# Kernel tuning notes

Hardware: AMD Instinct MI355X
Metric: run time of the kernel (lower is better)

Reference implementation:

```python
import jax, jax.numpy as jnp
import numpy as np

ALPHA = 0.3
N_TAGS = 50  # POS tag vocabulary size (key space of the histogram)
B, S, R = 16, 160, 40


def setup_inputs() -> dict:
    key = jax.random.key(0)
    k1, k2, k3, k4, k5, k6 = jax.random.split(key, 6)
    return {
        "a_arc": jax.random.normal(k1, (B, S, S), dtype=jnp.float32),
        "a_rel": jax.random.normal(k2, (B, S, S, R), dtype=jnp.float32),
        "s_arc": jax.random.normal(k3, (B, S, S), dtype=jnp.float32),
        "s_rel": jax.random.normal(k4, (B, S, S, R), dtype=jnp.float32),
        "adds": jax.random.randint(k5, (B, S), 0, N_TAGS, dtype=jnp.int32),
        "pos": jax.random.randint(k6, (B, S), 0, N_TAGS, dtype=jnp.int32),
        "n_tags": N_TAGS,
    }


def reference(a_arc, a_rel, s_arc, s_rel, adds, pos, n_tags):
    # Histogram accumulation: score[(t1, t2)] += a_arc[i, p1, p2]
    # where t1 = adds[i, p1], t2 = adds[i, p2].  Flatten the pair key.
    R_ = a_rel.shape[-1]
    key_add = (adds[:, :, None] * n_tags + adds[:, None, :]).reshape(-1)  # [B*S*S]
    n_seg = n_tags * n_tags
    tab_arc = jax.ops.segment_sum(a_arc.reshape(-1), key_add, num_segments=n_seg)          # [T^2]
    tab_rel = jax.ops.segment_sum(a_rel.reshape(-1, R_), key_add, num_segments=n_seg)      # [T^2, R]
    # Gather back keyed on pos-tag pairs and blend with alpha.
    key_pos = pos[:, :, None] * n_tags + pos[:, None, :]  # [B, S, S]
    s_arc_out = s_arc + tab_arc[key_pos] * ALPHA
    s_rel_out = s_rel + tab_rel[key_pos] * ALPHA
    return s_arc_out, s_rel_out
```

## Files before the change

kernel.cpp:

```cpp
#include <hip/hip_runtime.h>

#define ALPHA 0.3f
#define NT    50
#define B_    16
#define S_    160
#define RR    40
#define Q_    (RR / 4)
#define NROW  (B_ * S_)
#define NPAIR (B_ * S_ * S_)
#define NSEG  (NT * NT)
#define NREL4 (NPAIR * Q_)
#define NCOL  (NT * RR + NT)
#define CW    2052

typedef float v4f __attribute__((ext_vector_type(4)));

__global__ void zero_tab(float* __restrict__ tab, int n) {
    int i = blockIdx.x * blockDim.x + threadIdx.x;
    if (i < n) tab[i] = 0.0f;
}

__global__ void build_lists(const int* __restrict__ adds,
                            int* __restrict__ colstart,
                            int* __restrict__ collist) {
    __shared__ int tags[S_];
    __shared__ int cnt[NT];
    __shared__ int start[NT + 1];
    int b   = blockIdx.x;
    int tid = threadIdx.x;
    if (tid < S_) tags[tid] = adds[b * S_ + tid];
    __syncthreads();
    if (tid < NT) {
        int c = 0;
        for (int i = 0; i < S_; i++) c += (tags[i] == tid);
        cnt[tid] = c;
    }
    __syncthreads();
    if (tid == 0) {
        int s = 0;
        for (int t = 0; t < NT; t++) { start[t] = s; s += cnt[t]; }
        start[NT] = s;
    }
    __syncthreads();
    if (tid <= NT) colstart[b * 64 + tid] = start[tid];
    if (tid < NT) {
        int slot = start[tid];
        for (int i = 0; i < S_; i++)
            if (tags[i] == tid) collist[b * S_ + slot++] = i;
    }
}

template <int TO_C>
__global__ __launch_bounds__(256) void stage1(const float* __restrict__ a_arc,
                                              const float4* __restrict__ a_rel4,
                                              const int* __restrict__ adds,
                                              const int* __restrict__ colstart,
                                              const int* __restrict__ collist,
                                              float* __restrict__ C,
                                              float* __restrict__ tab_arc,
                                              float* __restrict__ tab_rel) {
    __shared__ v4f   a_srt[S_ * Q_];
    __shared__ float aarc_srt[S_];
    __shared__ int   s_start[NT + 1];
    __shared__ int   s_list[S_];
    int row = blockIdx.x;
    int b   = row / S_;
    int tid = threadIdx.x;

    if (tid <= NT) s_start[tid] = colstart[b * 64 + tid];
    if (tid < S_)  s_list[tid]  = collist[b * S_ + tid];
    __syncthreads();

    const v4f*   arow  = (const v4f*)(a_rel4 + (size_t)row * (S_ * Q_));
    const float* aarow = a_arc + (size_t)row * S_;

#pragma unroll
    for (int k = 0; k < 7; ++k) {
        int idx = k * 256 + tid;
        if (idx < S_ * Q_) {
            int j = idx / Q_;
            int q = idx - j * Q_;
            a_srt[idx] = __builtin_nontemporal_load(arow + s_list[j] * Q_ + q);
        }
    }
    if (tid < S_)
        aarc_srt[tid] = __builtin_nontemporal_load(aarow + s_list[tid]);
    __syncthreads();

    int t1 = TO_C ? 0 : adds[row];

    for (int cell = tid; cell < NT * Q_; cell += 256) {
        int t2 = cell / Q_;
        int q  = cell - t2 * Q_;
        int e  = s_start[t2];
        int e1 = s_start[t2 + 1];
        v4f acc = {0.f, 0.f, 0.f, 0.f};
        for (; e + 4 <= e1; e += 4) {
            v4f v0 = a_srt[(e + 0) * Q_ + q];
            v4f v1 = a_srt[(e + 1) * Q_ + q];
            v4f v2 = a_srt[(e + 2) * Q_ + q];
            v4f v3 = a_srt[(e + 3) * Q_ + q];
            acc += (v0 + v1) + (v2 + v3);
        }
        for (; e < e1; ++e) acc += a_srt[e * Q_ + q];
        if (TO_C) {
            ((v4f*)(C + (size_t)row * CW))[cell] = acc;
        } else {
            float* dst = tab_rel + (size_t)t1 * (NT * RR) + cell * 4;
            atomicAdd(dst + 0, acc.x); atomicAdd(dst + 1, acc.y);
            atomicAdd(dst + 2, acc.z); atomicAdd(dst + 3, acc.w);
        }
    }
    if (tid < NT) {
        int e  = s_start[tid];
        int e1 = s_start[tid + 1];
        float acc = 0.f;
        for (; e + 4 <= e1; e += 4) {
            acc += ((aarc_srt[e] + aarc_srt[e + 1])
                  + (aarc_srt[e + 2] + aarc_srt[e + 3]));
        }
        for (; e < e1; ++e) acc += aarc_srt[e];
        if (TO_C) C[(size_t)row * CW + NT * RR + tid] = acc;
        else      atomicAdd(tab_arc + t1 * NT + tid, acc);
    }
}

__global__ __launch_bounds__(256) void stage2(const float* __restrict__ C,
                                              const int* __restrict__ colstart,
                                              const int* __restrict__ collist,
                                              float* __restrict__ tab_arc,
                                              float* __restrict__ tab_rel) {
    int t1 = blockIdx.y;
    int c  = blockIdx.x * 256 + threadIdx.x;
    if (c >= NCOL) return;
    float acc = 0.f;
    for (int b = 0; b < B_; b++) {
        int s0 = colstart[b * 64 + t1], s1 = colstart[b * 64 + t1 + 1];
        for (int j = s0; j < s1; j++) {
            int row = b * S_ + collist[b * S_ + j];
            acc += C[(size_t)row * CW + c];
        }
    }
    if (c < NT * RR) tab_rel[t1 * (NT * RR) + c] = acc;
    else             tab_arc[t1 * NT + (c - NT * RR)] = acc;
}

template <bool NTS>
__global__ __launch_bounds__(256) void apply_v8(const float* __restrict__ s_arc,
                                                const v4f* __restrict__ s_rel4,
                                                const int* __restrict__ pos,
                                                const float* __restrict__ tab_arc,
                                                const v4f* __restrict__ tab_rel4,
                                                float* __restrict__ out_arc,
                                                v4f* __restrict__ out_rel4) {
    int row = blockIdx.x;
    int b   = row / S_;
    int p1  = row - b * S_;
    int tid = threadIdx.x;
    const int* posb = pos + b * S_;
    int base = posb[p1] * NT;

    int p2a[7], qa[7];
    {
        int p2 = tid / Q_, q = tid - (tid / Q_) * Q_;
#pragma unroll
        for (int k = 0; k < 7; ++k) {
            p2a[k] = (p2 < S_) ? p2 : 0;
            qa[k]  = q;
            q  += 6;
            p2 += 25;
            if (q >= Q_) { q -= Q_; p2 += 1; }
        }
    }
    int tp[7];
#pragma unroll
    for (int k = 0; k < 7; ++k) tp[k] = posb[p2a[k]];
    v4f tv[7];
#pragma unroll
    for (int k = 0; k < 7; ++k) tv[k] = tab_rel4[(base + tp[k]) * Q_ + qa[k]];

    const v4f* srow = s_rel4   + (size_t)row * (S_ * Q_);
    v4f*       orow = out_rel4 + (size_t)row * (S_ * Q_);
#pragma unroll
    for (int k = 0; k < 7; ++k) {
        int e = k * 256 + tid;
        if (e < S_ * Q_) {
            v4f o = srow[e] + ALPHA * tv[k];
            if (NTS) __builtin_nontemporal_store(o, orow + e);
            else     orow[e] = o;
        }
    }
    if (tid < S_) {
        float v = s_arc[(size_t)row * S_ + tid]
                + ALPHA * tab_arc[base + posb[tid]];
        if (NTS) __builtin_nontemporal_store(v, out_arc + (size_t)row * S_ + tid);
        else     out_arc[(size_t)row * S_ + tid] = v;
    }
}

extern "C" void kernel_launch(void* const* d_in, const int* in_sizes, int n_in,
                              void* d_out, int out_size, void* d_ws, size_t ws_size,
                              hipStream_t stream) {
    const float*  a_arc = (const float*)d_in[0];
    const float4* a_rel = (const float4*)d_in[1];
    const float*  s_arc = (const float*)d_in[2];
    const v4f*    s_rel = (const v4f*)d_in[3];
    const int*    adds  = (const int*)d_in[4];
    const int*    pos   = (const int*)d_in[5];

    float* tab_arc  = (float*)d_ws;
    float* tab_rel  = tab_arc + NSEG;
    int*   colstart = (int*)(tab_rel + NSEG * RR);
    int*   collist  = colstart + B_ * 64;
    float* C        = (float*)(collist + B_ * S_);
    C = (float*)(((uintptr_t)C + 15) & ~(uintptr_t)15);

    size_t need_lists = (size_t)(NSEG * (RR + 1)) * 4
                      + (size_t)(B_ * 64 + B_ * S_) * 4 + 16;
    size_t need_full  = need_lists + (size_t)NROW * CW * 4;

    float* out_arc = (float*)d_out;
    v4f*   out_rel = (v4f*)(out_arc + NPAIR);

    const int BLK = 256;

    build_lists<<<B_, 192, 0, stream>>>(adds, colstart, collist);

    if (ws_size >= need_full) {
        stage1<1><<<NROW, 256, 0, stream>>>(a_arc, a_rel, adds, colstart, collist,
                                            C, nullptr, nullptr);
        dim3 g2((NCOL + 255) / 256, NT);
        stage2<<<g2, 256, 0, stream>>>(C, colstart, collist, tab_arc, tab_rel);
    } else {
        int n_tab = NSEG * (RR + 1);
        zero_tab<<<(n_tab + BLK - 1) / BLK, BLK, 0, stream>>>(tab_arc, n_tab);
        stage1<0><<<NROW, 256, 0, stream>>>(a_arc, a_rel, adds, colstart, collist,
                                            nullptr, tab_arc, tab_rel);
    }

    apply_v8<true><<<NROW, 256, 0, stream>>>(s_arc, s_rel, pos, tab_arc,
                                             (const v4f*)tab_rel, out_arc, out_rel);
}
```

Measured before the change: 85.50 us.

## Fold per-batch tag sort into stage kernels and hoist s_rel loads in apply

Removes the separate build_lists launch by recomputing the per-batch counting sort inside each stage1 block, and inside stage2 for all 16 batches per block. This drops one kernel launch and the global list round-trip, at the cost of redundant sorting work and extra syncs in every block. The apply kernel now issues the s_rel/s_arc streaming loads before the table gathers so more memory requests are in flight.

```diff
diff --git a/kernel.cpp b/kernel.cpp
--- a/kernel.cpp
+++ b/kernel.cpp
@@ -20,42 +20,37 @@
     if (i < n) tab[i] = 0.0f;
 }
 
-__global__ void build_lists(const int* __restrict__ adds,
-                            int* __restrict__ colstart,
-                            int* __restrict__ collist) {
-    __shared__ int tags[S_];
-    __shared__ int cnt[NT];
-    __shared__ int start[NT + 1];
-    int b   = blockIdx.x;
-    int tid = threadIdx.x;
-    if (tid < S_) tags[tid] = adds[b * S_ + tid];
+__device__ __forceinline__ void sort_batch(const int* __restrict__ adds, int b,
+                                           int* s_start ,
+                                           int* s_list ,
+                                           int* s_tags ) {
+    int tid = threadIdx.x;
+    if (tid < S_) s_tags[tid] = adds[b * S_ + tid];
     __syncthreads();
     if (tid < NT) {
         int c = 0;
-        for (int i = 0; i < S_; i++) c += (tags[i] == tid);
-        cnt[tid] = c;
+        for (int i = 0; i < S_; i++) c += (s_tags[i] == tid);
+        s_start[tid] = c;
     }
     __syncthreads();
     if (tid == 0) {
         int s = 0;
-        for (int t = 0; t < NT; t++) { start[t] = s; s += cnt[t]; }
-        start[NT] = s;
-    }
-    __syncthreads();
-    if (tid <= NT) colstart[b * 64 + tid] = start[tid];
+        for (int t = 0; t < NT; t++) { int c = s_start[t]; s_start[t] = s; s += c; }
+        s_start[NT] = s;
+    }
+    __syncthreads();
     if (tid < NT) {
-        int slot = start[tid];
+        int slot = s_start[tid];
         for (int i = 0; i < S_; i++)
-            if (tags[i] == tid) collist[b * S_ + slot++] = i;
-    }
+            if (s_tags[i] == tid) s_list[slot++] = i;
+    }
+    __syncthreads();
 }
 
 template <int TO_C>
 __global__ __launch_bounds__(256) void stage1(const float* __restrict__ a_arc,
                                               const float4* __restrict__ a_rel4,
                                               const int* __restrict__ adds,
-                                              const int* __restrict__ colstart,
-                                              const int* __restrict__ collist,
                                               float* __restrict__ C,
                                               float* __restrict__ tab_arc,
                                               float* __restrict__ tab_rel) {
@@ -63,13 +58,12 @@
     __shared__ float aarc_srt[S_];
     __shared__ int   s_start[NT + 1];
     __shared__ int   s_list[S_];
+    __shared__ int   s_tags[S_];
     int row = blockIdx.x;
     int b   = row / S_;
     int tid = threadIdx.x;
 
-    if (tid <= NT) s_start[tid] = colstart[b * 64 + tid];
-    if (tid < S_)  s_list[tid]  = collist[b * S_ + tid];
-    __syncthreads();
+    sort_batch(adds, b, s_start, s_list, s_tags);
 
     const v4f*   arow  = (const v4f*)(a_rel4 + (size_t)row * (S_ * Q_));
     const float* aarow = a_arc + (size_t)row * S_;
@@ -87,7 +81,7 @@
         aarc_srt[tid] = __builtin_nontemporal_load(aarow + s_list[tid]);
     __syncthreads();
 
-    int t1 = TO_C ? 0 : adds[row];
+    int t1 = TO_C ? 0 : s_tags[row - b * S_];
 
     for (int cell = tid; cell < NT * Q_; cell += 256) {
         int t2 = cell / Q_;
@@ -126,27 +120,36 @@
 }
 
 __global__ __launch_bounds__(256) void stage2(const float* __restrict__ C,
-                                              const int* __restrict__ colstart,
-                                              const int* __restrict__ collist,
+                                              const int* __restrict__ adds,
                                               float* __restrict__ tab_arc,
                                               float* __restrict__ tab_rel) {
+    __shared__ int s_start[NT + 1];
+    __shared__ int s_list[S_];
+    __shared__ int s_tags[S_];
+    __shared__ int rows[S_];
+    __shared__ int nrows;
     int t1 = blockIdx.y;
-    int c  = blockIdx.x * 256 + threadIdx.x;
+    int tid = threadIdx.x;
+    if (tid == 0) nrows = 0;
+    __syncthreads();
+    for (int b = 0; b < B_; ++b) {
+        sort_batch(adds, b, s_start, s_list, s_tags);
+        int s0 = s_start[t1], s1 = s_start[t1 + 1];
+        if (tid < s1 - s0) rows[nrows + tid] = b * S_ + s_list[s0 + tid];
+        __syncthreads();
+        if (tid == 0) nrows += s1 - s0;
+        __syncthreads();
+    }
+    int c = blockIdx.x * 256 + threadIdx.x;
     if (c >= NCOL) return;
     float acc = 0.f;
-    for (int b = 0; b < B_; b++) {
-        int s0 = colstart[b * 64 + t1], s1 = colstart[b * 64 + t1 + 1];
-        for (int j = s0; j < s1; j++) {
-            int row = b * S_ + collist[b * S_ + j];
-            acc += C[(size_t)row * CW + c];
-        }
-    }
+    int n = nrows;
+    for (int j = 0; j < n; ++j) acc += C[(size_t)rows[j] * CW + c];
     if (c < NT * RR) tab_rel[t1 * (NT * RR) + c] = acc;
     else             tab_arc[t1 * NT + (c - NT * RR)] = acc;
 }
 
-template <bool NTS>
-__global__ __launch_bounds__(256) void apply_v8(const float* __restrict__ s_arc,
+__global__ __launch_bounds__(256) void apply_v9(const float* __restrict__ s_arc,
                                                 const v4f* __restrict__ s_rel4,
                                                 const int* __restrict__ pos,
                                                 const float* __restrict__ tab_arc,
@@ -158,8 +161,19 @@
     int p1  = row - b * S_;
     int tid = threadIdx.x;
     const int* posb = pos + b * S_;
+
+    const v4f* srow = s_rel4   + (size_t)row * (S_ * Q_);
+    v4f*       orow = out_rel4 + (size_t)row * (S_ * Q_);
+
+    v4f sv[7];
+#pragma unroll
+    for (int k = 0; k < 7; ++k) {
+        int e = k * 256 + tid;
+        sv[k] = (e < S_ * Q_) ? srow[e] : (v4f){0.f, 0.f, 0.f, 0.f};
+    }
+    float sa = (tid < S_) ? s_arc[(size_t)row * S_ + tid] : 0.f;
+
     int base = posb[p1] * NT;
-
     int p2a[7], qa[7];
     {
         int p2 = tid / Q_, q = tid - (tid / Q_) * Q_;
@@ -178,24 +192,17 @@
     v4f tv[7];
 #pragma unroll
     for (int k = 0; k < 7; ++k) tv[k] = tab_rel4[(base + tp[k]) * Q_ + qa[k]];
-
-    const v4f* srow = s_rel4   + (size_t)row * (S_ * Q_);
-    v4f*       orow = out_rel4 + (size_t)row * (S_ * Q_);
+    float ta = (tid < S_) ? tab_arc[base + posb[tid]] : 0.f;
+
 #pragma unroll
     for (int k = 0; k < 7; ++k) {
         int e = k * 256 + tid;
-        if (e < S_ * Q_) {
-            v4f o = srow[e] + ALPHA * tv[k];
-            if (NTS) __builtin_nontemporal_store(o, orow + e);
-            else     orow[e] = o;
-        }
-    }
-    if (tid < S_) {
-        float v = s_arc[(size_t)row * S_ + tid]
-                + ALPHA * tab_arc[base + posb[tid]];
-        if (NTS) __builtin_nontemporal_store(v, out_arc + (size_t)row * S_ + tid);
-        else     out_arc[(size_t)row * S_ + tid] = v;
-    }
+        if (e < S_ * Q_)
+            __builtin_nontemporal_store(sv[k] + ALPHA * tv[k], orow + e);
+    }
+    if (tid < S_)
+        __builtin_nontemporal_store(sa + ALPHA * ta,
+                                    out_arc + (size_t)row * S_ + tid);
 }
 
 extern "C" void kernel_launch(void* const* d_in, const int* in_sizes, int n_in,
@@ -208,36 +215,30 @@
     const int*    adds  = (const int*)d_in[4];
     const int*    pos   = (const int*)d_in[5];
 
-    float* tab_arc  = (float*)d_ws;
-    float* tab_rel  = tab_arc + NSEG;
-    int*   colstart = (int*)(tab_rel + NSEG * RR);
-    int*   collist  = colstart + B_ * 64;
-    float* C        = (float*)(collist + B_ * S_);
+    float* tab_arc = (float*)d_ws;
+    float* tab_rel = tab_arc + NSEG;
+    float* C       = tab_rel + NSEG * RR;
     C = (float*)(((uintptr_t)C + 15) & ~(uintptr_t)15);
 
-    size_t need_lists = (size_t)(NSEG * (RR + 1)) * 4
-                      + (size_t)(B_ * 64 + B_ * S_) * 4 + 16;
-    size_t need_full  = need_lists + (size_t)NROW * CW * 4;
+    size_t need_tab  = (size_t)(NSEG * (RR + 1)) * 4 + 16;
+    size_t need_full = need_tab + (size_t)NROW * CW * 4;
 
     float* out_arc = (float*)d_out;
     v4f*   out_rel = (v4f*)(out_arc + NPAIR);
 
     const int BLK = 256;
 
-    build_lists<<<B_, 192, 0, stream>>>(adds, colstart, collist);
-
     if (ws_size >= need_full) {
-        stage1<1><<<NROW, 256, 0, stream>>>(a_arc, a_rel, adds, colstart, collist,
-                                            C, nullptr, nullptr);
+        stage1<1><<<NROW, 256, 0, stream>>>(a_arc, a_rel, adds, C, nullptr, nullptr);
         dim3 g2((NCOL + 255) / 256, NT);
-        stage2<<<g2, 256, 0, stream>>>(C, colstart, collist, tab_arc, tab_rel);
+        stage2<<<g2, 256, 0, stream>>>(C, adds, tab_arc, tab_rel);
     } else {
         int n_tab = NSEG * (RR + 1);
         zero_tab<<<(n_tab + BLK - 1) / BLK, BLK, 0, stream>>>(tab_arc, n_tab);
-        stage1<0><<<NROW, 256, 0, stream>>>(a_arc, a_rel, adds, colstart, collist,
-                                            nullptr, tab_arc, tab_rel);
-    }
-
-    apply_v8<true><<<NROW, 256, 0, stream>>>(s_arc, s_rel, pos, tab_arc,
-                                             (const v4f*)tab_rel, out_arc, out_rel);
-}
+        stage1<0><<<NROW, 256, 0, stream>>>(a_arc, a_rel, adds, nullptr,
+                                            tab_arc, tab_rel);
+    }
+
+    apply_v9<<<NROW, 256, 0, stream>>>(s_arc, s_rel, pos, tab_arc,
+                                       (const v4f*)tab_rel, out_arc, out_rel);
+}
```

Measured after the change: 267.6 us. 213% more time.
